# Kernel tuning notes

Measured on AMD Instinct MI355X. Metric: run time of the kernel, lower is better.

## Reference

```python
import jax, jax.numpy as jnp
import numpy as np
from jax import lax


def loo_max(x):
    """Leave-one-out max over axis 1. x: (N, L, D) -> (N, L, D).
    Equivalent to torch's repeat + strip_main_diagonal + max(dim=2) without the
    (N, L, L, D) intermediate: for position i the LOO max is top1 unless i is
    the (unique chosen) argmax, in which case it is top2. With duplicates the
    second top-k value equals top1, so the result is still exact.
    """
    xt = jnp.swapaxes(x, 1, 2)                 # (N, D, L)
    top2, _ = lax.top_k(xt, 2)                 # (N, D, 2)
    amax = jnp.argmax(xt, axis=-1)             # (N, D)
    idx = jnp.arange(x.shape[1])[None, :, None]  # (1, L, 1)
    top1 = top2[..., 0][:, None, :]            # (N, 1, D)
    second = top2[..., 1][:, None, :]          # (N, 1, D)
    return jnp.where(idx == amax[:, None, :], second, top1)


def cross_max(y, from_length):
    """Plain max-pool over axis 1 of y, broadcast to (N, from_length, D)."""
    m = jnp.max(y, axis=1)                     # (N, D)
    return jnp.broadcast_to(m[:, None, :], (y.shape[0], from_length, y.shape[2]))


def setup_inputs() -> dict:
    key = jax.random.key(0)
    ks = jax.random.split(key, 6)
    N, L0, L1, D = 16, 2048, 1024, 128
    H = D + 2 * D  # in_dim + sum(in_dims) = 384
    scale = 1.0 / np.sqrt(H)
    return {
        "x0": jax.random.normal(ks[0], (N, L0, D), jnp.float32),
        "x1": jax.random.normal(ks[1], (N, L1, D), jnp.float32),
        "W0": jax.random.normal(ks[2], (D, H), jnp.float32) * scale,
        "b0": jax.random.normal(ks[3], (D,), jnp.float32) * scale,
        "W1": jax.random.normal(ks[4], (D, H), jnp.float32) * scale,
        "b1": jax.random.normal(ks[5], (D,), jnp.float32) * scale,
    }


def reference(x0, x1, W0, b0, W1, b1):
    L0, L1 = x0.shape[1], x1.shape[1]
    # group 0: [x0 | LOO-max(x0) | max(x1) broadcast] -> linear
    c0 = jnp.concatenate([x0, loo_max(x0), cross_max(x1, L0)], axis=-1)  # (N, L0, 384)
    y0 = jnp.einsum('nlh,oh->nlo', c0, W0) + b0                           # (N, L0, 128)
    # group 1: [x1 | max(x0) broadcast | LOO-max(x1)] -> linear
    c1 = jnp.concatenate([x1, cross_max(x0, L1), loo_max(x1)], axis=-1)  # (N, L1, 384)
    y1 = jnp.einsum('nlh,oh->nlo', c1, W1) + b1                           # (N, L1, 128)
    return (y0, y1)
```

## Files before the change

kernel.cpp:

```cpp
#include <hip/hip_runtime.h>
#include <hip/hip_bf16.h>

#define N_  16
#define L0_ 2048
#define L1_ 1024
#define D_  128
#define H_  384

#define PMQ_0 0
#define PMQ_1 262144
#define BASE_ 393216
#define WBF_  397312
#define HCNT_ 413696
#define HLIST_ 414464
#define XBF_  655360

typedef float  floatx4  __attribute__((ext_vector_type(4)));
typedef __bf16 bf16x8   __attribute__((ext_vector_type(8)));
typedef unsigned short ushortx8 __attribute__((ext_vector_type(8)));
typedef unsigned short ushortx4 __attribute__((ext_vector_type(4)));

__device__ __forceinline__ unsigned short f2bf(float f) {
  union { float f; unsigned int u; } v; v.f = f;
  unsigned int u = v.u;
  return (unsigned short)((u + 0x7fffu + ((u >> 16) & 1u)) >> 16);
}

__global__ __launch_bounds__(256) void stats_kernel(
    const float* __restrict__ x0, const float* __restrict__ x1,
    const float* __restrict__ W0, const float* __restrict__ W1,
    float* __restrict__ ws) {
  __shared__ float sm1[8][128], sm2[8][128];
  __shared__ int   sam[8][128];
  int bid = blockIdx.x, tid = threadIdx.x;

  if (bid >= 768) {
    int g = bid - 768;
    const float* W = g ? W1 : W0;
    unsigned short* wbf = (unsigned short*)(ws + WBF_) + g * 16384;
#pragma unroll 4
    for (int it = 0; it < 64; it++) {
      int f = tid + 256 * it;
      wbf[f] = f2bf(W[(size_t)(f >> 7) * H_ + (f & 127)]);
    }
    return;
  }

  const float* x; int n, chunk, L; floatx4* pmq;
  unsigned short* xbf;
  if (bid < 512) {
    x = x0; n = bid >> 5; chunk = bid & 31; L = L0_;
    pmq = (floatx4*)(ws + PMQ_0);
    xbf = (unsigned short*)(ws + XBF_);
  } else {
    int b = bid - 512;
    x = x1; n = b >> 4; chunk = b & 15; L = L1_;
    pmq = (floatx4*)(ws + PMQ_1);
    xbf = (unsigned short*)(ws + XBF_) + (size_t)N_ * L0_ * D_;
  }
  int q = tid & 31, sub = tid >> 5;
  int lbase = chunk * 64 + sub * 8;
  const float* xp = x + (size_t)(n * L + lbase) * D_ + q * 4;
  unsigned short* xbp = xbf + (size_t)(n * L + lbase) * D_ + q * 4;

  float m1[4], m2[4]; int am[4];
#pragma unroll
  for (int j = 0; j < 4; j++) { m1[j] = -3.4e38f; m2[j] = -3.4e38f; am[j] = 0; }
#pragma unroll
  for (int r = 0; r < 8; r++) {
    floatx4 v = __builtin_nontemporal_load((const floatx4*)(xp + (size_t)r * D_));
    ushortx4 bv = { f2bf(v[0]), f2bf(v[1]), f2bf(v[2]), f2bf(v[3]) };
    *(ushortx4*)(xbp + (size_t)r * D_) = bv;
    int l = lbase + r;
#pragma unroll
    for (int j = 0; j < 4; j++) {
      float vj = v[j];
      if (vj > m1[j]) { m2[j] = m1[j]; m1[j] = vj; am[j] = l; }
      else if (vj > m2[j]) m2[j] = vj;
    }
  }
#pragma unroll
  for (int j = 0; j < 4; j++) {
    int d = q * 4 + j;
    sm1[sub][d] = m1[j]; sm2[sub][d] = m2[j]; sam[sub][d] = am[j];
  }
  __syncthreads();
  if (tid < 128) {
    int d = tid;
    float M1 = sm1[0][d], M2 = sm2[0][d]; int AM = sam[0][d];
#pragma unroll
    for (int s = 1; s < 8; s++) {
      float c1 = sm1[s][d];
      if (c1 > M1) { M2 = fmaxf(M1, sm2[s][d]); M1 = c1; AM = sam[s][d]; }
      else M2 = fmaxf(M2, c1);
    }
    floatx4 outv = { M1, M2, __int_as_float(AM), 0.f };
    pmq[(chunk * N_ + n) * D_ + d] = outv;
  }
}

__global__ __launch_bounds__(256) void prep_kernel(
    const float* __restrict__ W0, const float* __restrict__ b0,
    const float* __restrict__ W1, const float* __restrict__ b1,
    float* __restrict__ ws) {
  __shared__ float t1a[128], t1b[128], sdl[128], bpart[128];
  __shared__ int   sam2[128], scnt[32];
  int bid = blockIdx.x, tid = threadIdx.x;
  int g = bid >> 4, n = bid & 15;
  const float* W = g ? W1 : W0;
  const float* bias = g ? b1 : b0;

  if (tid < 32) scnt[tid] = 0;

  if (tid < 128) {
    int d = tid;
    const floatx4* pmq = (const floatx4*)(ws + PMQ_0);
    floatx4 v = pmq[n * D_ + d];
    float M1 = v[0], M2 = v[1]; int AM = __float_as_int(v[2]);
#pragma unroll 8
    for (int c = 1; c < 32; c++) {
      floatx4 u = pmq[(c * N_ + n) * D_ + d];
      float c1 = u[0];
      if (c1 > M1) { M2 = fmaxf(M1, u[1]); M1 = c1; AM = __float_as_int(u[2]); }
      else M2 = fmaxf(M2, c1);
    }
    t1a[d] = M1;
    if (g == 0) { sdl[d] = M2 - M1; sam2[d] = AM; }
  } else {
    int d = tid - 128;
    const floatx4* pmq = (const floatx4*)(ws + PMQ_1);
    floatx4 v = pmq[n * D_ + d];
    float M1 = v[0], M2 = v[1]; int AM = __float_as_int(v[2]);
#pragma unroll 8
    for (int c = 1; c < 16; c++) {
      floatx4 u = pmq[(c * N_ + n) * D_ + d];
      float c1 = u[0];
      if (c1 > M1) { M2 = fmaxf(M1, u[1]); M1 = c1; AM = __float_as_int(u[2]); }
      else M2 = fmaxf(M2, c1);
    }
    t1b[d] = M1;
    if (g == 1) { sdl[d] = M2 - M1; sam2[d] = AM; }
  }
  __syncthreads();

  int o = tid & 127, half = tid >> 7;
  {
    const float* wr = W + (size_t)o * H_ + 128 + half * 128;
    const float* tv = half ? t1b : t1a;
    float bsum = 0.f;
#pragma unroll 4
    for (int d = 0; d < 128; d += 4) {
      float4 wv = *(const float4*)(wr + d);
      bsum += tv[d] * wv.x + tv[d + 1] * wv.y + tv[d + 2] * wv.z + tv[d + 3] * wv.w;
    }
    if (half) { bpart[o] = bsum; }
    __syncthreads();
    if (!half) ws[BASE_ + (g * N_ + n) * D_ + o] = bias[o] + bsum + bpart[o];
  }

  if (tid < 128) {
    int d = tid; int am = sam2[d]; float dl = sdl[d];
    int t = am >> 6;
    int slot = atomicAdd(&scnt[t], 1);
    int tile = (g == 0) ? (n * 32 + t) : (512 + n * 16 + t);
    int* hl = (int*)ws + HLIST_ + tile * 256;
    hl[slot * 2]     = (am & 63) | (d << 8);
    hl[slot * 2 + 1] = __float_as_int(dl);
  }
  __syncthreads();
  int tcount = g ? 16 : 32;
  if (tid < tcount) {
    int tile = (g == 0) ? (n * 32 + tid) : (512 + n * 16 + tid);
    ((int*)ws)[HCNT_ + tile] = scnt[tid];
  }
}

__global__ __launch_bounds__(256, 3) void gemm_kernel(
    const float* __restrict__ W0, const float* __restrict__ W1,
    float* __restrict__ out, const float* __restrict__ ws) {
  int bid = blockIdx.x, tid = threadIdx.x;
  int g, n, r0, L; const float* W; float* y; const unsigned short* xbf;
  if (bid < 512) {
    g = 0; n = bid >> 5; r0 = (bid & 31) << 6; L = L0_; W = W0; y = out;
    xbf = (const unsigned short*)(ws + XBF_);
  } else {
    int b = bid - 512; g = 1; n = b >> 4; r0 = (b & 15) << 6; L = L1_; W = W1;
    y = out + (size_t)N_ * L0_ * D_;
    xbf = (const unsigned short*)(ws + XBF_) + (size_t)N_ * L0_ * D_;
  }

  int w = tid >> 6, lane = tid & 63, lm = lane & 15, lq = lane >> 4;
  int rsub = (w & 1) << 5, cw = (w >> 1) << 6;

  int hc = ((const int*)ws)[HCNT_ + bid];
  const int* hl = (const int*)ws + HLIST_ + bid * 256;

  const unsigned short* wbf = (const unsigned short*)(ws + WBF_) + g * 16384;
  const unsigned short* xb = xbf + (size_t)(n * L + r0 + rsub) * D_;

  bf16x8 af[2][4];
  bf16x8 bfr[4][4];
#pragma unroll
  for (int kk = 0; kk < 4; kk++) {
    int ko = kk * 32 + lq * 8;
#pragma unroll
    for (int i = 0; i < 2; i++)
      af[i][kk] = __builtin_bit_cast(bf16x8,
          *(const ushortx8*)(xb + (size_t)(i * 16 + lm) * D_ + ko));
#pragma unroll
    for (int j = 0; j < 4; j++)
      bfr[j][kk] = __builtin_bit_cast(bf16x8,
          *(const ushortx8*)&wbf[(cw + j * 16 + lm) * 128 + ko]);
  }

  floatx4 acc[2][4];
#pragma unroll
  for (int i = 0; i < 2; i++)
#pragma unroll
    for (int j = 0; j < 4; j++) acc[i][j] = (floatx4){0.f, 0.f, 0.f, 0.f};

#pragma unroll
  for (int kk = 0; kk < 4; kk++)
#pragma unroll
    for (int i = 0; i < 2; i++)
#pragma unroll
      for (int j = 0; j < 4; j++)
        acc[i][j] = __builtin_amdgcn_mfma_f32_16x16x32_bf16(
            bfr[j][kk], af[i][kk], acc[i][j], 0, 0, 0);

  int off = 128 + (g << 7);
  for (int k = 0; k < hc; k++) {
    int e = hl[2 * k]; float dl = __int_as_float(hl[2 * k + 1]);
    int row = e & 63, d = e >> 8;
#pragma unroll
    for (int i = 0; i < 2; i++) {
      if (row == rsub + i * 16 + lm) {
#pragma unroll
        for (int j = 0; j < 4; j++)
#pragma unroll
          for (int r = 0; r < 4; r++)
            acc[i][j][r] += dl * W[(size_t)(cw + j * 16 + lq * 4 + r) * H_ + off + d];
      }
    }
  }

  const float* bp = ws + BASE_ + (g * N_ + n) * D_;
  float* yb = y + (size_t)(n * L + r0 + rsub) * D_;
#pragma unroll
  for (int i = 0; i < 2; i++)
#pragma unroll
    for (int j = 0; j < 4; j++) {
      floatx4 bbj = *(const floatx4*)&bp[cw + j * 16 + lq * 4];
      floatx4 v = acc[i][j] + bbj;
      __builtin_nontemporal_store(v,
          (floatx4*)&yb[(size_t)(i * 16 + lm) * D_ + cw + j * 16 + lq * 4]);
    }
}

extern "C" void kernel_launch(void* const* d_in, const int* in_sizes, int n_in,
                              void* d_out, int out_size, void* d_ws, size_t ws_size,
                              hipStream_t stream) {
  const float* x0 = (const float*)d_in[0];
  const float* x1 = (const float*)d_in[1];
  const float* W0 = (const float*)d_in[2];
  const float* b0 = (const float*)d_in[3];
  const float* W1 = (const float*)d_in[4];
  const float* b1 = (const float*)d_in[5];
  float* out = (float*)d_out;
  float* ws  = (float*)d_ws;

  hipLaunchKernelGGL(stats_kernel, dim3(770), dim3(256), 0, stream, x0, x1, W0, W1, ws);
  hipLaunchKernelGGL(prep_kernel,  dim3(32),  dim3(256), 0, stream, W0, b0, W1, b1, ws);
  hipLaunchKernelGGL(gemm_kernel,  dim3(768), dim3(256), 0, stream, W0, W1, out, ws);
}
```

Baseline: 112.9 us.

## Fuse stats, prep and GEMM into one cooperative persistent kernel

Replaces the three separate kernel launches with a single cooperative kernel of 512 blocks that uses grid-wide syncs between the stats, prep/weight-conversion and GEMM phases. Each block handles one tile, and blocks below 256 take a second tile so the original 768 work items are still covered. The aim is to remove launch gaps and inter-kernel drain between phases. In exchange it adds grid sync and threadfence costs, leaves load imbalance because only half the blocks do two tiles, and relies on all 512 blocks being co-resident, which the launch bound of 2 waves per EU is meant to allow.

```diff
diff --git a/kernel.cpp b/kernel.cpp
--- a/kernel.cpp
+++ b/kernel.cpp
@@ -1,5 +1,8 @@
 #include <hip/hip_runtime.h>
 #include <hip/hip_bf16.h>
+#include <hip/hip_cooperative_groups.h>
+
+namespace cg = cooperative_groups;
 
 #define N_  16
 #define L0_ 2048
@@ -26,26 +29,11 @@
   return (unsigned short)((u + 0x7fffu + ((u >> 16) & 1u)) >> 16);
 }
 
-__global__ __launch_bounds__(256) void stats_kernel(
+__device__ __forceinline__ void stats_tile(
+    int bid, int tid,
     const float* __restrict__ x0, const float* __restrict__ x1,
-    const float* __restrict__ W0, const float* __restrict__ W1,
-    float* __restrict__ ws) {
-  __shared__ float sm1[8][128], sm2[8][128];
-  __shared__ int   sam[8][128];
-  int bid = blockIdx.x, tid = threadIdx.x;
-
-  if (bid >= 768) {
-    int g = bid - 768;
-    const float* W = g ? W1 : W0;
-    unsigned short* wbf = (unsigned short*)(ws + WBF_) + g * 16384;
-#pragma unroll 4
-    for (int it = 0; it < 64; it++) {
-      int f = tid + 256 * it;
-      wbf[f] = f2bf(W[(size_t)(f >> 7) * H_ + (f & 127)]);
-    }
-    return;
-  }
-
+    float* __restrict__ ws,
+    float (&sm1)[8][128], float (&sm2)[8][128], int (&sam)[8][128]) {
   const float* x; int n, chunk, L; floatx4* pmq;
   unsigned short* xbf;
   if (bid < 512) {
@@ -99,13 +87,13 @@
   }
 }
 
-__global__ __launch_bounds__(256) void prep_kernel(
+__device__ __forceinline__ void prep_tile(
+    int bid, int tid,
     const float* __restrict__ W0, const float* __restrict__ b0,
     const float* __restrict__ W1, const float* __restrict__ b1,
-    float* __restrict__ ws) {
-  __shared__ float t1a[128], t1b[128], sdl[128], bpart[128];
-  __shared__ int   sam2[128], scnt[32];
-  int bid = blockIdx.x, tid = threadIdx.x;
+    float* __restrict__ ws,
+    float (&t1a)[128], float (&t1b)[128], float (&sdl)[128],
+    float (&bpart)[128], int (&sam2)[128], int (&scnt)[32]) {
   int g = bid >> 4, n = bid & 15;
   const float* W = g ? W1 : W0;
   const float* bias = g ? b1 : b0;
@@ -175,10 +163,22 @@
   }
 }
 
-__global__ __launch_bounds__(256, 3) void gemm_kernel(
+__device__ __forceinline__ void wconv_tile(
+    int g, int tid, const float* __restrict__ W0, const float* __restrict__ W1,
+    float* __restrict__ ws) {
+  const float* W = g ? W1 : W0;
+  unsigned short* wbf = (unsigned short*)(ws + WBF_) + g * 16384;
+#pragma unroll 4
+  for (int it = 0; it < 64; it++) {
+    int f = tid + 256 * it;
+    wbf[f] = f2bf(W[(size_t)(f >> 7) * H_ + (f & 127)]);
+  }
+}
+
+__device__ __forceinline__ void gemm_tile(
+    int bid, int tid,
     const float* __restrict__ W0, const float* __restrict__ W1,
     float* __restrict__ out, const float* __restrict__ ws) {
-  int bid = blockIdx.x, tid = threadIdx.x;
   int g, n, r0, L; const float* W; float* y; const unsigned short* xbf;
   if (bid < 512) {
     g = 0; n = bid >> 5; r0 = (bid & 31) << 6; L = L0_; W = W0; y = out;
@@ -255,6 +255,39 @@
       __builtin_nontemporal_store(v,
           (floatx4*)&yb[(size_t)(i * 16 + lm) * D_ + cw + j * 16 + lq * 4]);
     }
+}
+
+__global__ __launch_bounds__(256, 2) void fused_kernel(
+    const float* __restrict__ x0, const float* __restrict__ x1,
+    const float* __restrict__ W0, const float* __restrict__ b0,
+    const float* __restrict__ W1, const float* __restrict__ b1,
+    float* __restrict__ out, float* __restrict__ ws) {
+  __shared__ float sm1[8][128], sm2[8][128];
+  __shared__ int   sam[8][128];
+  __shared__ float t1a[128], t1b[128], sdl[128], bpart[128];
+  __shared__ int   sam2[128], scnt[32];
+
+  int bid = blockIdx.x, tid = threadIdx.x;
+  cg::grid_group grid = cg::this_grid();
+
+  stats_tile(bid, tid, x0, x1, ws, sm1, sm2, sam);
+  if (bid < 256) {
+    __syncthreads();
+    stats_tile(512 + bid, tid, x0, x1, ws, sm1, sm2, sam);
+  }
+  __threadfence();
+  grid.sync();
+
+  if (bid < 32)
+    prep_tile(bid, tid, W0, b0, W1, b1, ws, t1a, t1b, sdl, bpart, sam2, scnt);
+  else if (bid < 34)
+    wconv_tile(bid - 32, tid, W0, W1, ws);
+  __threadfence();
+  grid.sync();
+
+  gemm_tile(bid, tid, W0, W1, out, ws);
+  if (bid < 256)
+    gemm_tile(512 + bid, tid, W0, W1, out, ws);
 }
 
 extern "C" void kernel_launch(void* const* d_in, const int* in_sizes, int n_in,
@@ -269,7 +302,8 @@
   float* out = (float*)d_out;
   float* ws  = (float*)d_ws;
 
-  hipLaunchKernelGGL(stats_kernel, dim3(770), dim3(256), 0, stream, x0, x1, W0, W1, ws);
-  hipLaunchKernelGGL(prep_kernel,  dim3(32),  dim3(256), 0, stream, W0, b0, W1, b1, ws);
-  hipLaunchKernelGGL(gemm_kernel,  dim3(768), dim3(256), 0, stream, W0, W1, out, ws);
-}
+  void* args[] = { (void*)&x0, (void*)&x1, (void*)&W0, (void*)&b0,
+                   (void*)&W1, (void*)&b1, (void*)&out, (void*)&ws };
+  hipLaunchCooperativeKernel((const void*)fused_kernel, dim3(512), dim3(256),
+                             args, 0u, stream);
+}
```

Result: slower. 336.0 us (+197.6%).
